# Kernel optimization log

Hardware: AMD Instinct MI355X
Metric: run time of the kernel (lower is better)

The kernel has to match this reference:

```python
import jax, jax.numpy as jnp
import numpy as np

C_Z = 128
C_HIDDEN = 128
N_RES = 384
B = 1
EPS = 1e-5


def _layernorm(x, w, b):
    mu = jnp.mean(x, axis=-1, keepdims=True)
    var = jnp.mean(jnp.square(x - mu), axis=-1, keepdims=True)
    return (x - mu) * jax.lax.rsqrt(var + EPS) * w + b


def setup_inputs() -> dict:
    key = jax.random.key(0)
    ks = jax.random.split(key, 16)
    s_z = 1.0 / np.sqrt(C_Z)
    s_h = 1.0 / np.sqrt(C_HIDDEN)
    return {
        "z": jax.random.normal(ks[0], (B, N_RES, N_RES, C_Z), dtype=jnp.float32),
        "mask": jnp.ones((B, N_RES, N_RES), dtype=jnp.float32),
        "ln_in_w": jnp.ones((C_Z,), jnp.float32),
        "ln_in_b": jnp.zeros((C_Z,), jnp.float32),
        "a_g_w": jax.random.normal(ks[1], (C_HIDDEN, C_Z), jnp.float32) * s_z,
        "a_g_b": jnp.zeros((C_HIDDEN,), jnp.float32),
        "a_p_w": jax.random.normal(ks[2], (C_HIDDEN, C_Z), jnp.float32) * s_z,
        "a_p_b": jnp.zeros((C_HIDDEN,), jnp.float32),
        "b_g_w": jax.random.normal(ks[3], (C_HIDDEN, C_Z), jnp.float32) * s_z,
        "b_g_b": jnp.zeros((C_HIDDEN,), jnp.float32),
        "b_p_w": jax.random.normal(ks[4], (C_HIDDEN, C_Z), jnp.float32) * s_z,
        "b_p_b": jnp.zeros((C_HIDDEN,), jnp.float32),
        "g_w": jax.random.normal(ks[5], (C_Z, C_Z), jnp.float32) * s_z,
        "g_b": jnp.zeros((C_Z,), jnp.float32),
        "ln_out_w": jnp.ones((C_HIDDEN,), jnp.float32),
        "ln_out_b": jnp.zeros((C_HIDDEN,), jnp.float32),
        "z_w": jax.random.normal(ks[6], (C_Z, C_HIDDEN), jnp.float32) * s_h,
        "z_b": jnp.zeros((C_Z,), jnp.float32),
    }


def reference(z, mask, ln_in_w, ln_in_b, a_g_w, a_g_b, a_p_w, a_p_b,
              b_g_w, b_g_b, b_p_w, b_p_b, g_w, g_b,
              ln_out_w, ln_out_b, z_w, z_b):
    # z: [B, N, N, c_z]; mask: [B, N, N]
    m = mask[..., None]
    zn = _layernorm(z, ln_in_w, ln_in_b)
    # gated projections (fused LN+GEMM+sigmoid*mul in the Triton kernel)
    a = m * jax.nn.sigmoid(jnp.einsum("bijc,hc->bijh", zn, a_g_w) + a_g_b) \
          * (jnp.einsum("bijc,hc->bijh", zn, a_p_w) + a_p_b)
    b = m * jax.nn.sigmoid(jnp.einsum("bijc,hc->bijh", zn, b_g_w) + b_g_b) \
          * (jnp.einsum("bijc,hc->bijh", zn, b_p_w) + b_p_b)
    # outgoing triangle update: contract over third node k, per channel
    x = jnp.einsum("bikh,bjkh->bijh", a, b)
    # output path: sigmoid(gate(zn)) * linear_z(LN_out(x))
    xn = _layernorm(x, ln_out_w, ln_out_b)
    gate = jax.nn.sigmoid(jnp.einsum("bijc,oc->bijo", zn, g_w) + g_b)
    out = gate * (jnp.einsum("bijh,oh->bijo", xn, z_w) + z_b)
    return out
```

## Files before the change

kernel.cpp:

```cpp
#include <hip/hip_runtime.h>

#define NRES 384
#define CD   128
#define MTOT (NRES*NRES)

typedef unsigned short u16;
typedef __bf16 bf16x8 __attribute__((ext_vector_type(8)));
typedef float  f32x16 __attribute__((ext_vector_type(16)));

static __device__ __forceinline__ u16 f2bf(float f) {
  __bf16 b = (__bf16)f;
  return __builtin_bit_cast(u16, b);
}
static __device__ __forceinline__ float bf2f(u16 v) {
  return __uint_as_float(((unsigned)v) << 16);
}
static __device__ __forceinline__ float sigmoidf(float x) {
  return __builtin_amdgcn_rcpf(1.0f + __expf(-x));
}

static __device__ __forceinline__ void gl16(const void* g, void* l) {
  __builtin_amdgcn_global_load_lds(
      (const __attribute__((address_space(1))) void*)g,
      (__attribute__((address_space(3))) void*)l, 16, 0, 0);
}

__global__ void k_cvt_w(const float* w0, const float* w1, const float* w2,
                        const float* w3, const float* w4, const float* w5,
                        u16* wb) {
  int i = blockIdx.x * 256 + threadIdx.x;
  int which = blockIdx.x >> 6;
  const float* src = (which == 0) ? w0 : (which == 1) ? w1 : (which == 2) ? w2
                   : (which == 3) ? w3 : (which == 4) ? w4 : w5;
  wb[i] = f2bf(src[i & 16383]);
}

__global__ __launch_bounds__(256) void k_ln_in(const float* __restrict__ z,
                                               const float* __restrict__ w,
                                               const float* __restrict__ b,
                                               u16* __restrict__ zn) {
  int wv = threadIdx.x >> 6, lane = threadIdx.x & 63;
  float2 wv2 = ((const float2*)w)[lane];
  float2 bv2 = ((const float2*)b)[lane];
  for (int rr = 0; rr < 4; ++rr) {
    size_t row = (size_t)blockIdx.x * 16 + wv * 4 + rr;
    float2 v = ((const float2*)(z + row * CD))[lane];
    float s = v.x + v.y;
#pragma unroll
    for (int off = 32; off >= 1; off >>= 1) s += __shfl_xor(s, off);
    float mu = s * (1.0f / CD);
    float dx = v.x - mu, dy = v.y - mu;
    float vr = dx * dx + dy * dy;
#pragma unroll
    for (int off = 32; off >= 1; off >>= 1) vr += __shfl_xor(vr, off);
    float rs = rsqrtf(vr * (1.0f / CD) + 1e-5f);
    ushort2 o;
    o.x = f2bf(dx * rs * wv2.x + bv2.x);
    o.y = f2bf(dy * rs * wv2.y + bv2.y);
    ((ushort2*)(zn + row * CD))[lane] = o;
  }
}

__global__ __launch_bounds__(256) void k_proj(
    const u16* __restrict__ zn, const float* __restrict__ mask,
    const u16* __restrict__ wb,
    const float* __restrict__ agb, const float* __restrict__ apb,
    const float* __restrict__ bgb, const float* __restrict__ bpb,
    u16* __restrict__ a_out, u16* __restrict__ b_out) {
  int type = blockIdx.y;
  int m_base = blockIdx.x * 256;
  int t = threadIdx.x;
  int lane = t & 63;
  int wvu = __builtin_amdgcn_readfirstlane(t >> 6);
  int nl = lane & 31, s = lane >> 5;
  int h = wvu * 32 + nl;

  const u16* wgp = wb + (size_t)type * 32768;
  const u16* wpp = wgp + 16384;
  const float* bgp = (type == 0) ? agb : bgb;
  const float* bpp = (type == 0) ? apb : bpb;
  u16* outp = (type == 0) ? a_out : b_out;

  __shared__ u16 znt[3][64][128];
  __shared__ float bsl[2][128];

  if (t < 128) bsl[0][t] = bgp[t];
  else         bsl[1][t - 128] = bpp[t - 128];

  float mk0[4], mk1[4];
#pragma unroll
  for (int ms = 0; ms < 4; ++ms) {
    mk0[ms] = mask[m_base + ms * 64 + nl];
    mk1[ms] = mask[m_base + ms * 64 + 32 + nl];
  }

  bf16x8 wgf[8], wpf[8];
#pragma unroll
  for (int kk = 0; kk < 8; ++kk) {
    wgf[kk] = *(const bf16x8*)(wgp + h * CD + kk * 16 + s * 8);
    wpf[kk] = *(const bf16x8*)(wpp + h * CD + kk * 16 + s * 8);
  }

  int rl = lane >> 4, p16 = lane & 15;
#define STAGE_ZNT(mt, bf)                                                   \
  {                                                                         \
    _Pragma("unroll")                                                       \
    for (int j = 0; j < 4; ++j) {                                           \
      int row = wvu * 16 + j * 4 + rl;                                      \
      int gc = (p16 ^ (row & 7)) << 3;                                      \
      gl16(zn + (size_t)((mt) + row) * CD + gc, &znt[bf][wvu * 16 + j * 4][0]); \
    }                                                                       \
  }

  asm volatile("" ::: "memory");
  STAGE_ZNT(m_base, 0);
  asm volatile("" ::: "memory");
  STAGE_ZNT(m_base + 64, 1);
  asm volatile("" ::: "memory");

  asm volatile("s_waitcnt lgkmcnt(0)" ::: "memory");

#define PROJ_ITER(ms, buf, WAITINSN, STAGEIT, stbuf)                          \
  {                                                                           \
    asm volatile(WAITINSN ::: "memory");                                      \
    __builtin_amdgcn_s_barrier();                                             \
    asm volatile("" ::: "memory");                                            \
    f32x16 accg0, accg1, accp0, accp1;                                        \
    _Pragma("unroll")                                                         \
    for (int i = 0; i < 16; ++i) {                                            \
      accg0[i] = 0; accg1[i] = 0; accp0[i] = 0; accp1[i] = 0;                 \
    }                                                                         \
    _Pragma("unroll")                                                         \
    for (int kk = 0; kk < 8; ++kk) {                                          \
      int c = ((kk * 2 + s) ^ (nl & 7)) << 3;                                 \
      bf16x8 zf0 = *(const bf16x8*)&znt[buf][nl][c];                          \
      bf16x8 zf1 = *(const bf16x8*)&znt[buf][32 + nl][c];                     \
      accg0 = __builtin_amdgcn_mfma_f32_32x32x16_bf16(wgf[kk], zf0, accg0, 0, 0, 0); \
      accg1 = __builtin_amdgcn_mfma_f32_32x32x16_bf16(wgf[kk], zf1, accg1, 0, 0, 0); \
      accp0 = __builtin_amdgcn_mfma_f32_32x32x16_bf16(wpf[kk], zf0, accp0, 0, 0, 0); \
      accp1 = __builtin_amdgcn_mfma_f32_32x32x16_bf16(wpf[kk], zf1, accp1, 0, 0, 0); \
    }                                                                         \
    int mt = m_base + (ms) * 64;                                              \
    _Pragma("unroll")                                                         \
    for (int r = 0; r < 16; ++r) {                                            \
      int hh = wvu * 32 + (r & 3) + 8 * (r >> 2) + 4 * s;                     \
      float bg = bsl[0][hh], bp = bsl[1][hh];                                 \
      u16* rowp = outp + (size_t)hh * MTOT + mt + nl;                         \
      rowp[0]  = f2bf(mk0[ms] * sigmoidf(accg0[r] + bg) * (accp0[r] + bp));   \
      rowp[32] = f2bf(mk1[ms] * sigmoidf(accg1[r] + bg) * (accp1[r] + bp));   \
    }                                                                         \
    asm volatile("" ::: "memory");                                            \
    if (STAGEIT) STAGE_ZNT(m_base + ((ms) + 2) * 64, stbuf);                  \
    asm volatile("" ::: "memory");                                            \
  }

  PROJ_ITER(0, 0, "s_waitcnt vmcnt(4)", 1, 2);
  PROJ_ITER(1, 1, "s_waitcnt vmcnt(4)", 1, 0);
  PROJ_ITER(2, 2, "s_waitcnt vmcnt(4)", 0, 0);
  PROJ_ITER(3, 0, "s_waitcnt vmcnt(0)", 0, 0);
#undef PROJ_ITER
#undef STAGE_ZNT
}

__global__ __launch_bounds__(256) void k_tri(const u16* __restrict__ a,
                                             const u16* __restrict__ b,
                                             u16* __restrict__ x) {
  int h  = blockIdx.y;
  int tm = blockIdx.x / 3, tn = blockIdx.x % 3;
  int i0 = tm * 128, j0 = tn * 128;
  const u16* ah = a + (size_t)h * MTOT;
  const u16* bh = b + (size_t)h * MTOT;

  __shared__ u16 At[2][128][64];
  __shared__ u16 Bt[2][128][64];

  int lane = threadIdx.x & 63;
  int wvu = __builtin_amdgcn_readfirstlane(threadIdx.x >> 6);
  int nl = lane & 31, s = lane >> 5;
  int wr = wvu >> 1, wc = wvu & 1;
  int rl = lane >> 3, p8 = lane & 7;

  f32x16 acc[4];
#pragma unroll
  for (int q = 0; q < 4; ++q)
#pragma unroll
    for (int i = 0; i < 16; ++i) acc[q][i] = 0;

#define STAGE_TRI(bf, k0)                                                     \
  {                                                                           \
    _Pragma("unroll")                                                         \
    for (int j = 0; j < 4; ++j) {                                             \
      int row = wvu * 32 + j * 8 + rl;                                        \
      int gc = (p8 ^ (rl & 7)) << 3;                                          \
      gl16(ah + (size_t)(i0 + row) * NRES + (k0) + gc, &At[bf][wvu * 32 + j * 8][0]); \
      gl16(bh + (size_t)(j0 + row) * NRES + (k0) + gc, &Bt[bf][wvu * 32 + j * 8][0]); \
    }                                                                         \
  }

  STAGE_TRI(0, 0);
  __syncthreads();

  for (int kb = 0; kb < 6; ++kb) {
    int cur = kb & 1;
    if (kb < 5) STAGE_TRI(cur ^ 1, (kb + 1) * 64);
#pragma unroll
    for (int kk = 0; kk < 4; ++kk) {
      int c = ((kk * 2 + s) ^ (nl & 7)) << 3;
      bf16x8 af0 = *(const bf16x8*)&At[cur][wr * 64 + nl][c];
      bf16x8 af1 = *(const bf16x8*)&At[cur][wr * 64 + 32 + nl][c];
      bf16x8 bf0 = *(const bf16x8*)&Bt[cur][wc * 64 + nl][c];
      bf16x8 bf1 = *(const bf16x8*)&Bt[cur][wc * 64 + 32 + nl][c];
      acc[0] = __builtin_amdgcn_mfma_f32_32x32x16_bf16(af0, bf0, acc[0], 0, 0, 0);
      acc[1] = __builtin_amdgcn_mfma_f32_32x32x16_bf16(af0, bf1, acc[1], 0, 0, 0);
      acc[2] = __builtin_amdgcn_mfma_f32_32x32x16_bf16(af1, bf0, acc[2], 0, 0, 0);
      acc[3] = __builtin_amdgcn_mfma_f32_32x32x16_bf16(af1, bf1, acc[3], 0, 0, 0);
    }
    __syncthreads();
  }
#undef STAGE_TRI

  u16* xh = x + (size_t)h * MTOT;
#pragma unroll
  for (int msub = 0; msub < 2; ++msub)
#pragma unroll
    for (int nsub = 0; nsub < 2; ++nsub) {
      int j = j0 + wc * 64 + nsub * 32 + nl;
#pragma unroll
      for (int r = 0; r < 16; ++r) {
        int i = i0 + wr * 64 + msub * 32 + (r & 3) + 8 * (r >> 2) + 4 * s;
        xh[(size_t)i * NRES + j] = f2bf(acc[msub * 2 + nsub][r]);
      }
    }
}

__global__ __launch_bounds__(256) void k_out(
    const u16* __restrict__ x, const u16* __restrict__ zn,
    const u16* __restrict__ wb, const float* __restrict__ gb,
    const float* __restrict__ lnw, const float* __restrict__ lnb,
    const float* __restrict__ zb, float* __restrict__ out) {
  int m0 = blockIdx.x * 64;
  int t = threadIdx.x;
  int wv = t >> 6, lane = t & 63, nl = lane & 31, s = lane >> 5;
  int o = wv * 32 + nl;

  __shared__ u16 tile[64][136];

  const u16* gwp = wb + 4 * 16384;
  const u16* zwp = wb + 5 * 16384;

  bf16x8 gwf[8];
#pragma unroll
  for (int kk = 0; kk < 8; ++kk)
    gwf[kk] = *(const bf16x8*)(gwp + o * CD + kk * 16 + s * 8);

#pragma unroll
  for (int it = 0; it < 4; ++it) {
    int idx = it * 256 + t;
    int r = idx >> 4, c8 = idx & 15;
    *(uint4*)&tile[r][c8 * 8] =
        *(const uint4*)(zn + (size_t)(m0 + r) * CD + c8 * 8);
  }
  __syncthreads();

  f32x16 gacc[2];
#pragma unroll
  for (int i = 0; i < 16; ++i) { gacc[0][i] = 0; gacc[1][i] = 0; }
#pragma unroll
  for (int kk = 0; kk < 8; ++kk) {
    bf16x8 zf0 = *(const bf16x8*)&tile[nl][kk * 16 + s * 8];
    bf16x8 zf1 = *(const bf16x8*)&tile[32 + nl][kk * 16 + s * 8];
    gacc[0] = __builtin_amdgcn_mfma_f32_32x32x16_bf16(zf0, gwf[kk], gacc[0], 0, 0, 0);
    gacc[1] = __builtin_amdgcn_mfma_f32_32x32x16_bf16(zf1, gwf[kk], gacc[1], 0, 0, 0);
  }
  float gbv = gb[o];
  float gv[32];
#pragma unroll
  for (int ms = 0; ms < 2; ++ms)
#pragma unroll
    for (int r = 0; r < 16; ++r)
      gv[ms * 16 + r] = sigmoidf(gacc[ms][r] + gbv);
  __syncthreads();

  bf16x8 zwf[8];
#pragma unroll
  for (int kk = 0; kk < 8; ++kk)
    zwf[kk] = *(const bf16x8*)(zwp + o * CD + kk * 16 + s * 8);

#pragma unroll
  for (int ps = 0; ps < 2; ++ps) {
    int idx = ps * 256 + t;
    int hp = idx >> 3, mc = idx & 7;
    uint4 v0 = *(const uint4*)(x + (size_t)(2 * hp)     * MTOT + m0 + mc * 8);
    uint4 v1 = *(const uint4*)(x + (size_t)(2 * hp + 1) * MTOT + m0 + mc * 8);
    unsigned c0[4] = {v0.x, v0.y, v0.z, v0.w};
    unsigned c1[4] = {v1.x, v1.y, v1.z, v1.w};
#pragma unroll
    for (int q = 0; q < 4; ++q) {
      ushort2 lo, hi;
      lo.x = (u16)(c0[q] & 0xffffu); lo.y = (u16)(c1[q] & 0xffffu);
      hi.x = (u16)(c0[q] >> 16);     hi.y = (u16)(c1[q] >> 16);
      *(ushort2*)&tile[mc * 8 + 2 * q][2 * hp]     = lo;
      *(ushort2*)&tile[mc * 8 + 2 * q + 1][2 * hp] = hi;
    }
  }
  __syncthreads();

  int r = t >> 2, q = t & 3;
  float vals[32];
  float sum = 0;
#pragma unroll
  for (int j = 0; j < 32; ++j) { float v = bf2f(tile[r][q * 32 + j]); vals[j] = v; sum += v; }
  sum += __shfl_xor(sum, 1);
  sum += __shfl_xor(sum, 2);
  float mu = sum * (1.0f / CD);
  float var = 0;
#pragma unroll
  for (int j = 0; j < 32; ++j) { float d = vals[j] - mu; var += d * d; }
  var += __shfl_xor(var, 1);
  var += __shfl_xor(var, 2);
  float rs = rsqrtf(var * (1.0f / CD) + 1e-5f);
#pragma unroll
  for (int j = 0; j < 32; ++j) {
    int hh = q * 32 + j;
    tile[r][hh] = f2bf((vals[j] - mu) * rs * lnw[hh] + lnb[hh]);
  }
  __syncthreads();

  f32x16 acc[2];
#pragma unroll
  for (int i = 0; i < 16; ++i) { acc[0][i] = 0; acc[1][i] = 0; }
#pragma unroll
  for (int kk = 0; kk < 8; ++kk) {
    bf16x8 af0 = *(const bf16x8*)&tile[nl][kk * 16 + s * 8];
    bf16x8 af1 = *(const bf16x8*)&tile[32 + nl][kk * 16 + s * 8];
    acc[0] = __builtin_amdgcn_mfma_f32_32x32x16_bf16(af0, zwf[kk], acc[0], 0, 0, 0);
    acc[1] = __builtin_amdgcn_mfma_f32_32x32x16_bf16(af1, zwf[kk], acc[1], 0, 0, 0);
  }

  float zbv = zb[o];
#pragma unroll
  for (int ms = 0; ms < 2; ++ms)
#pragma unroll
    for (int rr = 0; rr < 16; ++rr) {
      int rowoff = (rr & 3) + 8 * (rr >> 2) + 4 * s;
      int mg = m0 + ms * 32 + rowoff;
      out[(size_t)mg * CD + o] = gv[ms * 16 + rr] * (acc[ms][rr] + zbv);
    }
}

extern "C" void kernel_launch(void* const* d_in, const int* in_sizes, int n_in,
                              void* d_out, int out_size, void* d_ws, size_t ws_size,
                              hipStream_t stream) {
  const float* z       = (const float*)d_in[0];
  const float* mask    = (const float*)d_in[1];
  const float* ln_in_w = (const float*)d_in[2];
  const float* ln_in_b = (const float*)d_in[3];
  const float* a_g_w   = (const float*)d_in[4];
  const float* a_g_b   = (const float*)d_in[5];
  const float* a_p_w   = (const float*)d_in[6];
  const float* a_p_b   = (const float*)d_in[7];
  const float* b_g_w   = (const float*)d_in[8];
  const float* b_g_b   = (const float*)d_in[9];
  const float* b_p_w   = (const float*)d_in[10];
  const float* b_p_b   = (const float*)d_in[11];
  const float* g_w     = (const float*)d_in[12];
  const float* g_b     = (const float*)d_in[13];
  const float* ln_o_w  = (const float*)d_in[14];
  const float* ln_o_b  = (const float*)d_in[15];
  const float* z_w     = (const float*)d_in[16];
  const float* z_b     = (const float*)d_in[17];
  float* out = (float*)d_out;

  const size_t SZ = (size_t)MTOT * CD * sizeof(u16);
  char* w = (char*)d_ws;
  u16* zn = (u16*)(w);
  u16* a  = (u16*)(w + SZ);
  u16* b  = (u16*)(w + 2 * SZ);
  u16* x  = (u16*)(w + 3 * SZ);
  u16* wb = (u16*)(w + 4 * SZ);
  (void)ws_size; (void)in_sizes; (void)n_in; (void)out_size;

  k_cvt_w<<<384, 256, 0, stream>>>(a_g_w, a_p_w, b_g_w, b_p_w, g_w, z_w, wb);
  k_ln_in<<<MTOT / 16, 256, 0, stream>>>(z, ln_in_w, ln_in_b, zn);
  k_proj<<<dim3(MTOT / 256, 2), 256, 0, stream>>>(zn, mask, wb,
      a_g_b, a_p_b, b_g_b, b_p_b, a, b);
  k_tri<<<dim3(9, 128), 256, 0, stream>>>(a, b, x);
  k_out<<<MTOT / 64, 256, 0, stream>>>(x, zn, wb, g_b, ln_o_w, ln_o_b, z_b, out);
}
```

Measured before the change: 284.9 us.

## Fold output LayerNorm into linear_z weights and prefetch loads early in k_out

The output LayerNorm affine is folded into the z_w weights (scaled by ln_out_w) plus per-output constants computed by a new tiny kernel. k_out now computes only per-row mean and rstd, using a single-pass sum and sum-of-squares, and applies them in the epilogue, so it no longer rewrites the normalized tile to LDS. Global loads of zn and x are issued up front to overlap with the gate GEMM, and __syncthreads is replaced by explicit waitcnt plus barrier. The single-pass variance is less numerically robust, and the GEMM now runs on un-normalized bf16 x values.

```diff
diff --git a/kernel.cpp b/kernel.cpp
--- a/kernel.cpp
+++ b/kernel.cpp
@@ -27,12 +27,31 @@
 
 __global__ void k_cvt_w(const float* w0, const float* w1, const float* w2,
                         const float* w3, const float* w4, const float* w5,
-                        u16* wb) {
+                        const float* lnw, u16* wb) {
   int i = blockIdx.x * 256 + threadIdx.x;
   int which = blockIdx.x >> 6;
   const float* src = (which == 0) ? w0 : (which == 1) ? w1 : (which == 2) ? w2
                    : (which == 3) ? w3 : (which == 4) ? w4 : w5;
-  wb[i] = f2bf(src[i & 16383]);
+  float v = src[i & 16383];
+  if (which == 5) v *= lnw[i & 127];
+  wb[i] = f2bf(v);
+}
+
+__global__ void k_c12(const float* __restrict__ zw, const float* __restrict__ lnw,
+                      const float* __restrict__ lnb, const float* __restrict__ zb,
+                      float2* __restrict__ c12) {
+  int o = blockIdx.x, l = threadIdx.x;
+  float2 v = ((const float2*)(zw + o * CD))[l];
+  float2 w = ((const float2*)lnw)[l];
+  float2 b = ((const float2*)lnb)[l];
+  float s1 = v.x * w.x + v.y * w.y;
+  float s2 = v.x * b.x + v.y * b.y;
+#pragma unroll
+  for (int off = 32; off >= 1; off >>= 1) {
+    s1 += __shfl_xor(s1, off);
+    s2 += __shfl_xor(s2, off);
+  }
+  if (l == 0) c12[o] = make_float2(s1, s2 + zb[o]);
 }
 
 __global__ __launch_bounds__(256) void k_ln_in(const float* __restrict__ z,
@@ -236,31 +255,46 @@
 __global__ __launch_bounds__(256) void k_out(
     const u16* __restrict__ x, const u16* __restrict__ zn,
     const u16* __restrict__ wb, const float* __restrict__ gb,
-    const float* __restrict__ lnw, const float* __restrict__ lnb,
-    const float* __restrict__ zb, float* __restrict__ out) {
+    const float2* __restrict__ c12, float* __restrict__ out) {
   int m0 = blockIdx.x * 64;
   int t = threadIdx.x;
   int wv = t >> 6, lane = t & 63, nl = lane & 31, s = lane >> 5;
   int o = wv * 32 + nl;
 
   __shared__ u16 tile[64][136];
+  __shared__ float2 stat[64];
 
   const u16* gwp = wb + 4 * 16384;
   const u16* zwp = wb + 5 * 16384;
 
+  uint4 znv[4];
+#pragma unroll
+  for (int it = 0; it < 4; ++it) {
+    int idx = it * 256 + t, r = idx >> 4, c8 = idx & 15;
+    znv[it] = *(const uint4*)(zn + (size_t)(m0 + r) * CD + c8 * 8);
+  }
   bf16x8 gwf[8];
 #pragma unroll
   for (int kk = 0; kk < 8; ++kk)
     gwf[kk] = *(const bf16x8*)(gwp + o * CD + kk * 16 + s * 8);
+  float gbv = gb[o];
+
+  int mc = t & 7;
+  uint4 xv0[2], xv1[2];
+#pragma unroll
+  for (int ps = 0; ps < 2; ++ps) {
+    int hp = (ps * 256 + t) >> 3;
+    xv0[ps] = *(const uint4*)(x + (size_t)(2 * hp)     * MTOT + m0 + mc * 8);
+    xv1[ps] = *(const uint4*)(x + (size_t)(2 * hp + 1) * MTOT + m0 + mc * 8);
+  }
 
 #pragma unroll
   for (int it = 0; it < 4; ++it) {
-    int idx = it * 256 + t;
-    int r = idx >> 4, c8 = idx & 15;
-    *(uint4*)&tile[r][c8 * 8] =
-        *(const uint4*)(zn + (size_t)(m0 + r) * CD + c8 * 8);
-  }
-  __syncthreads();
+    int idx = it * 256 + t, r = idx >> 4, c8 = idx & 15;
+    *(uint4*)&tile[r][c8 * 8] = znv[it];
+  }
+  asm volatile("s_waitcnt lgkmcnt(0)" ::: "memory");
+  __builtin_amdgcn_s_barrier();
 
   f32x16 gacc[2];
 #pragma unroll
@@ -272,14 +306,14 @@
     gacc[0] = __builtin_amdgcn_mfma_f32_32x32x16_bf16(zf0, gwf[kk], gacc[0], 0, 0, 0);
     gacc[1] = __builtin_amdgcn_mfma_f32_32x32x16_bf16(zf1, gwf[kk], gacc[1], 0, 0, 0);
   }
-  float gbv = gb[o];
   float gv[32];
 #pragma unroll
   for (int ms = 0; ms < 2; ++ms)
 #pragma unroll
     for (int r = 0; r < 16; ++r)
       gv[ms * 16 + r] = sigmoidf(gacc[ms][r] + gbv);
-  __syncthreads();
+  asm volatile("s_waitcnt lgkmcnt(0)" ::: "memory");
+  __builtin_amdgcn_s_barrier();
 
   bf16x8 zwf[8];
 #pragma unroll
@@ -288,12 +322,9 @@
 
 #pragma unroll
   for (int ps = 0; ps < 2; ++ps) {
-    int idx = ps * 256 + t;
-    int hp = idx >> 3, mc = idx & 7;
-    uint4 v0 = *(const uint4*)(x + (size_t)(2 * hp)     * MTOT + m0 + mc * 8);
-    uint4 v1 = *(const uint4*)(x + (size_t)(2 * hp + 1) * MTOT + m0 + mc * 8);
-    unsigned c0[4] = {v0.x, v0.y, v0.z, v0.w};
-    unsigned c1[4] = {v1.x, v1.y, v1.z, v1.w};
+    int hp = (ps * 256 + t) >> 3;
+    unsigned c0[4] = {xv0[ps].x, xv0[ps].y, xv0[ps].z, xv0[ps].w};
+    unsigned c1[4] = {xv1[ps].x, xv1[ps].y, xv1[ps].z, xv1[ps].w};
 #pragma unroll
     for (int q = 0; q < 4; ++q) {
       ushort2 lo, hi;
@@ -303,28 +334,30 @@
       *(ushort2*)&tile[mc * 8 + 2 * q + 1][2 * hp] = hi;
     }
   }
-  __syncthreads();
-
-  int r = t >> 2, q = t & 3;
-  float vals[32];
-  float sum = 0;
-#pragma unroll
-  for (int j = 0; j < 32; ++j) { float v = bf2f(tile[r][q * 32 + j]); vals[j] = v; sum += v; }
-  sum += __shfl_xor(sum, 1);
-  sum += __shfl_xor(sum, 2);
-  float mu = sum * (1.0f / CD);
-  float var = 0;
-#pragma unroll
-  for (int j = 0; j < 32; ++j) { float d = vals[j] - mu; var += d * d; }
-  var += __shfl_xor(var, 1);
-  var += __shfl_xor(var, 2);
-  float rs = rsqrtf(var * (1.0f / CD) + 1e-5f);
-#pragma unroll
-  for (int j = 0; j < 32; ++j) {
-    int hh = q * 32 + j;
-    tile[r][hh] = f2bf((vals[j] - mu) * rs * lnw[hh] + lnb[hh]);
-  }
-  __syncthreads();
+  asm volatile("s_waitcnt lgkmcnt(0)" ::: "memory");
+  __builtin_amdgcn_s_barrier();
+
+  {
+    int r = t >> 2, q = t & 3;
+    float sum = 0.0f, sq = 0.0f;
+#pragma unroll
+    for (int i = 0; i < 4; ++i) {
+      uint4 v = *(const uint4*)&tile[r][q * 32 + i * 8];
+      unsigned cc[4] = {v.x, v.y, v.z, v.w};
+#pragma unroll
+      for (int j = 0; j < 4; ++j) {
+        float a = bf2f((u16)(cc[j] & 0xffffu));
+        float b = bf2f((u16)(cc[j] >> 16));
+        sum += a + b; sq += a * a + b * b;
+      }
+    }
+    sum += __shfl_xor(sum, 1); sum += __shfl_xor(sum, 2);
+    sq  += __shfl_xor(sq, 1);  sq  += __shfl_xor(sq, 2);
+    float mu = sum * (1.0f / CD);
+    float var = sq * (1.0f / CD) - mu * mu;
+    float rs = rsqrtf(var + 1e-5f);
+    if (q == 0) stat[r] = make_float2(rs, rs * mu);
+  }
 
   f32x16 acc[2];
 #pragma unroll
@@ -336,15 +369,19 @@
     acc[0] = __builtin_amdgcn_mfma_f32_32x32x16_bf16(af0, zwf[kk], acc[0], 0, 0, 0);
     acc[1] = __builtin_amdgcn_mfma_f32_32x32x16_bf16(af1, zwf[kk], acc[1], 0, 0, 0);
   }
-
-  float zbv = zb[o];
+  asm volatile("s_waitcnt lgkmcnt(0)" ::: "memory");
+  __builtin_amdgcn_s_barrier();
+
+  float2 cc2 = c12[o];
 #pragma unroll
   for (int ms = 0; ms < 2; ++ms)
 #pragma unroll
     for (int rr = 0; rr < 16; ++rr) {
       int rowoff = (rr & 3) + 8 * (rr >> 2) + 4 * s;
-      int mg = m0 + ms * 32 + rowoff;
-      out[(size_t)mg * CD + o] = gv[ms * 16 + rr] * (acc[ms][rr] + zbv);
+      int row = ms * 32 + rowoff;
+      float2 st = stat[row];
+      out[(size_t)(m0 + row) * CD + o] =
+          gv[ms * 16 + rr] * (st.x * acc[ms][rr] - st.y * cc2.x + cc2.y);
     }
 }
 
@@ -378,12 +415,15 @@
   u16* b  = (u16*)(w + 2 * SZ);
   u16* x  = (u16*)(w + 3 * SZ);
   u16* wb = (u16*)(w + 4 * SZ);
+  float2* c12 = (float2*)(w + 4 * SZ + 6 * 16384 * sizeof(u16));
   (void)ws_size; (void)in_sizes; (void)n_in; (void)out_size;
 
-  k_cvt_w<<<384, 256, 0, stream>>>(a_g_w, a_p_w, b_g_w, b_p_w, g_w, z_w, wb);
+  k_cvt_w<<<384, 256, 0, stream>>>(a_g_w, a_p_w, b_g_w, b_p_w, g_w, z_w,
+                                   ln_o_w, wb);
+  k_c12<<<128, 64, 0, stream>>>(z_w, ln_o_w, ln_o_b, z_b, c12);
   k_ln_in<<<MTOT / 16, 256, 0, stream>>>(z, ln_in_w, ln_in_b, zn);
   k_proj<<<dim3(MTOT / 256, 2), 256, 0, stream>>>(zn, mask, wb,
       a_g_b, a_p_b, b_g_b, b_p_b, a, b);
   k_tri<<<dim3(9, 128), 256, 0, stream>>>(a, b, x);
-  k_out<<<MTOT / 64, 256, 0, stream>>>(x, zn, wb, g_b, ln_o_w, ln_o_b, z_b, out);
-}
+  k_out<<<MTOT / 64, 256, 0, stream>>>(x, zn, wb, g_b, c12, out);
+}
```

Result: faster. 274.9 us (-3.5%).
